# Kernel optimization log

Hardware: AMD Instinct MI355X
Metric: run time of the kernel (lower is better)

## Reference

```python
import jax, jax.numpy as jnp
import numpy as np

H = 16        # num_heads
LN_EPS = 1e-6

def _ln(x, w, b):
    mu = x.mean(-1, keepdims=True)
    var = ((x - mu) ** 2).mean(-1, keepdims=True)
    return (x - mu) * jax.lax.rsqrt(var + LN_EPS) * w + b

def setup_inputs():
    key = jax.random.key(0)
    ks = jax.random.split(key, 6)
    B, L, S, D = 2, 8192, 512, 1024
    std = 0.02
    return {
        "q_in": jax.random.normal(ks[0], (B, L, D), jnp.float32),
        "kv_in": jax.random.normal(ks[1], (B, S, D), jnp.float32),
        "qn_w": jnp.ones((D,), jnp.float32),
        "qn_b": jnp.zeros((D,), jnp.float32),
        "kvn_w": jnp.ones((D,), jnp.float32),
        "kvn_b": jnp.zeros((D,), jnp.float32),
        "Wq": jax.random.normal(ks[2], (D, D), jnp.float32) * std,
        "Wk": jax.random.normal(ks[3], (D, D), jnp.float32) * std,
        "Wv": jax.random.normal(ks[4], (D, D), jnp.float32) * std,
        "Wo": jax.random.normal(ks[5], (D, D), jnp.float32) * std,
        "bo": jnp.zeros((D,), jnp.float32),
        "gate": jnp.ones((1,), jnp.float32),
    }

def reference(q_in, kv_in, qn_w, qn_b, kvn_w, kvn_b, Wq, Wk, Wv, Wo, bo, gate):
    b, l, hid = q_in.shape
    s = kv_in.shape[1]
    d = hid // H
    scale = d ** -0.5
    q_x = _ln(q_in, qn_w, qn_b)
    kv_x = _ln(kv_in, kvn_w, kvn_b)
    # torch Linear: y = x @ W.T  (weights stored [out, in])
    q = (q_x @ Wq.T).reshape(b, l, H, d).transpose(0, 2, 1, 3)   # [b,H,l,d]
    k = (kv_x @ Wk.T).reshape(b, s, H, d).transpose(0, 2, 1, 3)  # [b,H,s,d]
    v = (kv_x @ Wv.T).reshape(b, s, H, d).transpose(0, 2, 1, 3)  # [b,H,s,d]
    logits = jnp.einsum('bhld,bhsd->bhls', q, k) * scale
    attn = jax.nn.softmax(logits, axis=-1)                       # [b,H,l,s]
    # no-grad diagnostics
    attn_d = jax.lax.stop_gradient(attn).astype(jnp.float32)
    ent_per_head = -(attn_d * jnp.log(attn_d + 1e-9)).sum(-1).mean(axis=(0, 2))  # [H]
    mean_entropy = ent_per_head.mean()
    head_entropy_std = ent_per_head.std()  # population std (unbiased=False)
    top_k = min(4, s)
    top_mass = jax.lax.top_k(attn_d, top_k)[0].sum(-1).mean()
    out = jnp.einsum('bhls,bhsd->bhld', attn, v)
    out = out.transpose(0, 2, 1, 3).reshape(b, l, hid)
    out = (out @ Wo.T + bo) * gate  # dropout=0 -> identity; gate broadcasts
    return (out, mean_entropy, head_entropy_std, top_mass, gate[0])
```

## Files before the change

kernel.cpp:

```cpp
#include <hip/hip_runtime.h>
#include <stdint.h>
#include <stddef.h>


typedef __attribute__((ext_vector_type(8))) short bf16x8;
typedef __attribute__((ext_vector_type(4))) float f32x4;
typedef __attribute__((ext_vector_type(16))) float f32x16;
typedef __attribute__((ext_vector_type(2))) unsigned int u32x2;

#define MFMA(a, b, c)   __builtin_amdgcn_mfma_f32_16x16x32_bf16((a), (b), (c), 0, 0, 0)
#define MFMA32(a, b, c) __builtin_amdgcn_mfma_f32_32x32x16_bf16((a), (b), (c), 0, 0, 0)
#define MED3(a, b, c)   __builtin_amdgcn_fmed3f((a), (b), (c))

__device__ __forceinline__ float bf2f(unsigned short u) {
  union { unsigned int ui; float f; } cv; cv.ui = ((unsigned int)u) << 16; return cv.f;
}
__device__ __forceinline__ unsigned short f2bf(float f) {
  union { float f; unsigned int ui; } cv; cv.f = f;
  unsigned int u = cv.ui;
  u = u + 0x7fffu + ((u >> 16) & 1u);
  return (unsigned short)(u >> 16);
}
__device__ __forceinline__ unsigned int pk2(float a, float b) {
  union { float f; unsigned int u; } ua, ub; ua.f = a; ub.f = b;
  return __builtin_amdgcn_perm(ub.u, ua.u, 0x07060302u);
}
__device__ __forceinline__ float ex2(float x) {
#if __has_builtin(__builtin_amdgcn_exp2f)
  return __builtin_amdgcn_exp2f(x);
#else
  float r; asm("v_exp_f32 %0, %1" : "=v"(r) : "v"(x)); return r;
#endif
}
__device__ __forceinline__ void pl32swap(unsigned int& a, unsigned int& b) {
#if __has_builtin(__builtin_amdgcn_permlane32_swap)
  u32x2 r = __builtin_amdgcn_permlane32_swap(a, b, false, false);
  a = r[0]; b = r[1];
#else
  asm volatile("v_permlane32_swap_b32 %0, %1" : "+v"(a), "+v"(b));
#endif
}
__device__ __forceinline__ bool is_fp32(const unsigned int* probe) {
  return probe[0] == 0x3F800000u;
}
__device__ __forceinline__ void gl2lds(const unsigned short* g, unsigned short* l) {
  __builtin_amdgcn_global_load_lds(
      (const __attribute__((address_space(1))) void*)(uintptr_t)g,
      (__attribute__((address_space(3))) void*)(unsigned int)(uintptr_t)l,
      16, 0, 0);
}

__device__ __forceinline__ size_t qf_addr(int qg, int d) {
  int b = qg >> 13, q = qg & 8191, h = d >> 6, dd = d & 63;
  int lane = (q & 31) | (((dd >> 3) & 1) << 5);
  return ((((size_t)(b * 16 + h) * 256 + (q >> 5)) * 4 + (dd >> 4)) * 64 + lane) * 8 + (dd & 7);
}
__device__ __forceinline__ size_t kf_addr(int r, int d) {
  int b = r >> 9, s = r & 511, h = d >> 6, dd = d & 63;
  int lane = (s & 31) | (((dd >> 3) & 1) << 5);
  return ((((size_t)(b * 16 + h) * 16 + (s >> 5)) * 4 + (dd >> 4)) * 64 + lane) * 8 + (dd & 7);
}
__device__ __forceinline__ size_t vf_addr(int r, int d) {
  int b = r >> 9, s = r & 511, h = d >> 6, dd = d & 63;
  int lane = (dd & 31) | (((s >> 3) & 1) << 5);
  return (((((size_t)(b * 16 + h) * 16 + (s >> 5)) * 2 + (dd >> 5)) * 2 + ((s >> 4) & 1)) * 64 + lane) * 8 + (s & 7);
}

__device__ __forceinline__ void ln_row_impl(
    bool f32, const void* __restrict__ xv, const void* __restrict__ wv,
    const void* __restrict__ bv, unsigned short* __restrict__ y,
    int row, int tid, float* rs, float* rs2)
{
  float v0, v1, v2, v3, w0, w1, w2, w3, b0, b1, b2, b3;
  if (f32) {
    float4 xr = *(const float4*)((const float*)xv + (size_t)row * 1024 + tid * 4);
    v0 = xr.x; v1 = xr.y; v2 = xr.z; v3 = xr.w;
    float4 wr = *(const float4*)((const float*)wv + tid * 4);
    w0 = wr.x; w1 = wr.y; w2 = wr.z; w3 = wr.w;
    float4 br = *(const float4*)((const float*)bv + tid * 4);
    b0 = br.x; b1 = br.y; b2 = br.z; b3 = br.w;
  } else {
    ushort4 xr = *(const ushort4*)((const unsigned short*)xv + (size_t)row * 1024 + tid * 4);
    v0 = bf2f(xr.x); v1 = bf2f(xr.y); v2 = bf2f(xr.z); v3 = bf2f(xr.w);
    ushort4 wr = *(const ushort4*)((const unsigned short*)wv + tid * 4);
    w0 = bf2f(wr.x); w1 = bf2f(wr.y); w2 = bf2f(wr.z); w3 = bf2f(wr.w);
    ushort4 br = *(const ushort4*)((const unsigned short*)bv + tid * 4);
    b0 = bf2f(br.x); b1 = bf2f(br.y); b2 = bf2f(br.z); b3 = bf2f(br.w);
  }
  float s  = v0 + v1 + v2 + v3;
  float s2 = v0*v0 + v1*v1 + v2*v2 + v3*v3;
  #pragma unroll
  for (int off = 32; off > 0; off >>= 1) {
    s  += __shfl_xor(s, off);
    s2 += __shfl_xor(s2, off);
  }
  if ((tid & 63) == 0) { rs[tid >> 6] = s; rs2[tid >> 6] = s2; }
  __syncthreads();
  s  = rs[0] + rs[1] + rs[2] + rs[3];
  s2 = rs2[0] + rs2[1] + rs2[2] + rs2[3];
  const float mean = s * (1.0f / 1024.0f);
  const float var  = s2 * (1.0f / 1024.0f) - mean * mean;
  const float rstd = 1.0f / sqrtf(var + 1e-6f);
  ushort4 o;
  o.x = f2bf((v0 - mean) * rstd * w0 + b0);
  o.y = f2bf((v1 - mean) * rstd * w1 + b1);
  o.z = f2bf((v2 - mean) * rstd * w2 + b2);
  o.w = f2bf((v3 - mean) * rstd * w3 + b3);
  *(ushort4*)(y + (size_t)row * 1024 + tid * 4) = o;
}

__global__ __launch_bounds__(256) void prep_all(
    const unsigned int* __restrict__ probe,
    const void* __restrict__ q_in, const void* __restrict__ qn_w,
    const void* __restrict__ qn_b, unsigned short* __restrict__ qx,
    const void* __restrict__ w0, const void* __restrict__ w1,
    const void* __restrict__ w2, const void* __restrict__ w3,
    unsigned short* __restrict__ wdst,
    const void* __restrict__ kv_in, const void* __restrict__ kvn_w,
    const void* __restrict__ kvn_b, unsigned short* __restrict__ kvx,
    const void* __restrict__ bo, const void* __restrict__ gate,
    unsigned short* __restrict__ bob, unsigned short* __restrict__ gateb,
    float* __restrict__ stats)
{
  __shared__ float rs[4], rs2[4];
  const bool f32 = is_fp32(probe);
  const int bx = blockIdx.x, tid = threadIdx.x;
  if (bx < 16384) {
    ln_row_impl(f32, q_in, qn_w, qn_b, qx, bx, tid, rs, rs2);
    return;
  }
  const int b2 = bx - 16384;
  if (b2 < 4096) {
    const int m = b2 >> 10;
    const void* src = (m == 0) ? w0 : (m == 1) ? w1 : (m == 2) ? w2 : w3;
    unsigned short* d = wdst + (size_t)m * 1048576;
    const int i = (b2 & 1023) * 1024 + tid * 4;
    ushort4 o;
    if (f32) {
      float4 v = *(const float4*)((const float*)src + i);
      o.x = f2bf(v.x); o.y = f2bf(v.y); o.z = f2bf(v.z); o.w = f2bf(v.w);
    } else {
      o = *(const ushort4*)((const unsigned short*)src + i);
    }
    *(ushort4*)(d + i) = o;
  } else if (b2 < 5120) {
    ln_row_impl(f32, kv_in, kvn_w, kvn_b, kvx, b2 - 4096, tid, rs, rs2);
  } else {
    ushort4 o;
    if (f32) {
      float4 v = *(const float4*)((const float*)bo + tid * 4);
      o.x = f2bf(v.x); o.y = f2bf(v.y); o.z = f2bf(v.z); o.w = f2bf(v.w);
    } else {
      o = *(const ushort4*)((const unsigned short*)bo + tid * 4);
    }
    *(ushort4*)(bob + tid * 4) = o;
    if (tid == 0)
      gateb[0] = f32 ? f2bf(((const float*)gate)[0]) : ((const unsigned short*)gate)[0];
    if (tid < 17) stats[tid] = 0.0f;
  }
}

template <int MODE>
__device__ __forceinline__ void gemm_core(
    const unsigned int* __restrict__ probe,
    const unsigned short* __restrict__ A, const unsigned short* __restrict__ B,
    void* __restrict__ Cv, int N, int K, int m0, int n0,
    const unsigned short* __restrict__ bias, const unsigned short* __restrict__ gate,
    unsigned short* As, unsigned short* Bs)
{
  const int tid = threadIdx.x;
  const int wave = tid >> 6, lane = tid & 63, ln = lane & 15, quad = lane >> 4;
  const int wm = (wave >> 1) * 64, wn = (wave & 1) * 64;
  f32x4 acc[4][4] = {};
  for (int k0 = 0; k0 < K; k0 += 64) {
    __syncthreads();
    #pragma unroll
    for (int i = 0; i < 4; i++) {
      int idx = tid + i * 256;
      int r = idx >> 3, ch = (idx & 7) * 8;
      gl2lds(A + (size_t)(m0 + r) * K + k0 + ch, As + r * 64 + ch);
      gl2lds(B + (size_t)(n0 + r) * K + k0 + ch, Bs + r * 64 + ch);
    }
    __syncthreads();
    #pragma unroll
    for (int kk = 0; kk < 64; kk += 32) {
      bf16x8 af[4], bfr[4];
      #pragma unroll
      for (int i = 0; i < 4; i++) {
        af[i]  = *(const bf16x8*)(As + (wm + i * 16 + ln) * 64 + kk + quad * 8);
        bfr[i] = *(const bf16x8*)(Bs + (wn + i * 16 + ln) * 64 + kk + quad * 8);
      }
      #pragma unroll
      for (int mi = 0; mi < 4; mi++)
        #pragma unroll
        for (int ni = 0; ni < 4; ni++)
          acc[mi][ni] = MFMA(af[mi], bfr[ni], acc[mi][ni]);
    }
  }
  const bool f32o = (MODE == 1) && is_fp32(probe);
  const float g = (MODE == 1) ? bf2f(gate[0]) : 1.0f;
  #pragma unroll
  for (int mi = 0; mi < 4; mi++) {
    #pragma unroll
    for (int ni = 0; ni < 4; ni++) {
      const int col = n0 + wn + ni * 16 + ln;
      const float badd = (MODE == 1) ? bf2f(bias[col]) : 0.0f;
      #pragma unroll
      for (int r = 0; r < 4; r++) {
        const int row = m0 + wm + mi * 16 + quad * 4 + r;
        const float val = (acc[mi][ni][r] + badd) * g;
        if (MODE == 1) {
          if (f32o) ((float*)Cv)[(size_t)row * N + col] = val;
          else ((unsigned short*)Cv)[(size_t)row * N + col] = f2bf(val);
        } else if (MODE == 2) {
          ((unsigned short*)Cv)[qf_addr(row, col)] = f2bf(val * 0.18033688f);
        } else {
          if (col < 1024) ((unsigned short*)Cv)[kf_addr(row, col)] = f2bf(val);
          else ((unsigned short*)Cv)[1048576 + vf_addr(row, col - 1024)] = f2bf(val);
        }
      }
    }
  }
}

template <int MODE>
__global__ __launch_bounds__(256, 3) void gemm_nt(
    const unsigned int* __restrict__ probe,
    const unsigned short* __restrict__ A, const unsigned short* __restrict__ B,
    void* __restrict__ Cv, int M, int N, int K,
    const unsigned short* __restrict__ bias, const unsigned short* __restrict__ gate)
{
  __shared__ unsigned short As[128 * 64];
  __shared__ unsigned short Bs[128 * 64];
  const int nbx = gridDim.x;
  const int nwg = nbx * gridDim.y;
  const int cpx = nwg >> 3;
  const int flat = blockIdx.y * nbx + blockIdx.x;
  const int swz = (flat & 7) * cpx + (flat >> 3);
  const int n0 = (swz % nbx) * 128;
  const int m0 = (swz / nbx) * 128;
  gemm_core<MODE>(probe, A, B, Cv, N, K, m0, n0, bias, gate, As, Bs);
}

__global__ __launch_bounds__(256, 3) void gemm_qkv(
    const unsigned int* __restrict__ probe,
    const unsigned short* __restrict__ qx, const unsigned short* __restrict__ kvx,
    const unsigned short* __restrict__ wcv,
    unsigned short* __restrict__ qfrag, unsigned short* __restrict__ kvfrag)
{
  __shared__ unsigned short As[128 * 64];
  __shared__ unsigned short Bs[128 * 64];
  const int flat = blockIdx.x;
  const int xcd = flat & 7, local = flat >> 3;
  if (local < 16) {
    const int id = xcd * 16 + local;
    gemm_core<5>(probe, kvx, wcv + 1048576, kvfrag, 2048, 1024,
                 (id >> 4) * 128, (id & 15) * 128, nullptr, nullptr, As, Bs);
  } else {
    const int id = xcd * 128 + (local - 16);
    gemm_core<2>(probe, qx, wcv, qfrag, 1024, 1024,
                 (id >> 3) * 128, (id & 7) * 128, nullptr, nullptr, As, Bs);
  }
}

#define TRK(T0, T1, T2, T3, L, SQ, IDX) {                                     \
    float x_ = S[IDX];                                                        \
    float o0 = T0, o1 = T1, o2 = T2;                                          \
    T0 = fmaxf(o0, x_); T1 = MED3(o0, o1, x_);                                \
    T2 = MED3(o1, o2, x_); T3 = MED3(o2, T3, x_);                             \
    float p_ = ex2(x_); L += p_; SQ = fmaf(p_, x_, SQ); S[IDX] = p_; }

#define MERGE4(A0, A1, A2, A3, B0, B1, B2, B3) {                              \
    float c0 = fmaxf(A0, B3), c1 = fmaxf(A1, B2);                             \
    float c2 = fmaxf(A2, B1), c3 = fmaxf(A3, B0);                             \
    float d0 = fmaxf(c0, c2), d2 = fminf(c0, c2);                             \
    float d1 = fmaxf(c1, c3), d3 = fminf(c1, c3);                             \
    A0 = fmaxf(d0, d1); A1 = fminf(d0, d1);                                   \
    A2 = fmaxf(d2, d3); A3 = fminf(d2, d3); }

__global__ __launch_bounds__(256, 3) void attn_kernel(
    const unsigned short* __restrict__ Qf, const unsigned short* __restrict__ Kf,
    const unsigned short* __restrict__ Vf, unsigned short* __restrict__ ctx,
    float* __restrict__ stats)
{
  __shared__ float red_e[4], red_t[4];
  const int tid = threadIdx.x;
  const int wave = tid >> 6, lane = tid & 63;
  const int qc = blockIdx.x & 63;
  const int bh = blockIdx.x >> 6;
  const int h = bh & 15, bb = bh >> 4;
  const int qt = qc * 4 + wave;

  const unsigned short* qfb = Qf + ((((size_t)bh * 256 + qt) * 4) * 64 + lane) * 8;
  const bf16x8 bq0 = *(const bf16x8*)(qfb);
  const bf16x8 bq1 = *(const bf16x8*)(qfb + 512);
  const bf16x8 bq2 = *(const bf16x8*)(qfb + 1024);
  const bf16x8 bq3 = *(const bf16x8*)(qfb + 1536);

  const unsigned short* kfb = Kf + ((size_t)bh * 64 * 64 + lane) * 8;
  const unsigned short* vfb = Vf + ((size_t)bh * 64 * 64 + lane) * 8;

  float l0 = 0.f, l1 = 0.f, l2 = 0.f, l3 = 0.f;
  float q0 = 0.f, q1 = 0.f, q2 = 0.f, q3 = 0.f;
  float ta0 = -1e30f, ta1 = -1e30f, ta2 = -1e30f, ta3 = -1e30f;
  float tb0 = -1e30f, tb1 = -1e30f, tb2 = -1e30f, tb3 = -1e30f;
  float tc0 = -1e30f, tc1 = -1e30f, tc2 = -1e30f, tc3 = -1e30f;
  float td0 = -1e30f, td1 = -1e30f, td2 = -1e30f, td3 = -1e30f;
  f32x16 Od0 = {}, Od1 = {};

  bf16x8 kf0 = *(const bf16x8*)(kfb);
  bf16x8 kf1 = *(const bf16x8*)(kfb + 512);
  bf16x8 kf2 = *(const bf16x8*)(kfb + 1024);
  bf16x8 kf3 = *(const bf16x8*)(kfb + 1536);

  for (int ch = 0; ch < 16; ch++) {
    const unsigned short* vp = vfb + (size_t)ch * 2048;
    const bf16x8 v00 = *(const bf16x8*)(vp);
    const bf16x8 v01 = *(const bf16x8*)(vp + 512);
    const bf16x8 v10 = *(const bf16x8*)(vp + 1024);
    const bf16x8 v11 = *(const bf16x8*)(vp + 1536);

    f32x16 S = {};
    __builtin_amdgcn_s_setprio(1);
    S = MFMA32(kf0, bq0, S);
    S = MFMA32(kf1, bq1, S);
    S = MFMA32(kf2, bq2, S);
    S = MFMA32(kf3, bq3, S);
    __builtin_amdgcn_s_setprio(0);

    {
      const unsigned short* kp = kfb + (size_t)(ch + 1) * 2048;
      kf0 = *(const bf16x8*)(kp);
      kf1 = *(const bf16x8*)(kp + 512);
      kf2 = *(const bf16x8*)(kp + 1024);
      kf3 = *(const bf16x8*)(kp + 1536);
    }

    TRK(ta0, ta1, ta2, ta3, l0, q0, 0)  TRK(tb0, tb1, tb2, tb3, l1, q1, 4)
    TRK(tc0, tc1, tc2, tc3, l2, q2, 8)  TRK(td0, td1, td2, td3, l3, q3, 12)
    TRK(ta0, ta1, ta2, ta3, l0, q0, 1)  TRK(tb0, tb1, tb2, tb3, l1, q1, 5)
    TRK(tc0, tc1, tc2, tc3, l2, q2, 9)  TRK(td0, td1, td2, td3, l3, q3, 13)
    TRK(ta0, ta1, ta2, ta3, l0, q0, 2)  TRK(tb0, tb1, tb2, tb3, l1, q1, 6)
    TRK(tc0, tc1, tc2, tc3, l2, q2, 10) TRK(td0, td1, td2, td3, l3, q3, 14)
    TRK(ta0, ta1, ta2, ta3, l0, q0, 3)  TRK(tb0, tb1, tb2, tb3, l1, q1, 7)
    TRK(tc0, tc1, tc2, tc3, l2, q2, 11) TRK(td0, td1, td2, td3, l3, q3, 15)

    unsigned int W0 = pk2(S[0],  S[1]),  W1 = pk2(S[2],  S[3]);
    unsigned int W2 = pk2(S[4],  S[5]),  W3 = pk2(S[6],  S[7]);
    unsigned int W4 = pk2(S[8],  S[9]),  W5 = pk2(S[10], S[11]);
    unsigned int W6 = pk2(S[12], S[13]), W7 = pk2(S[14], S[15]);
    pl32swap(W0, W2); pl32swap(W1, W3);
    pl32swap(W4, W6); pl32swap(W5, W7);
    union { unsigned int u[4]; bf16x8 v; } pb0, pb1;
    pb0.u[0] = W0; pb0.u[1] = W1; pb0.u[2] = W2; pb0.u[3] = W3;
    pb1.u[0] = W4; pb1.u[1] = W5; pb1.u[2] = W6; pb1.u[3] = W7;

    __builtin_amdgcn_s_setprio(1);
    Od0 = MFMA32(v00, pb0.v, Od0);
    Od0 = MFMA32(v01, pb1.v, Od0);
    Od1 = MFMA32(v10, pb0.v, Od1);
    Od1 = MFMA32(v11, pb1.v, Od1);
    __builtin_amdgcn_s_setprio(0);
  }

  MERGE4(ta0, ta1, ta2, ta3, tc0, tc1, tc2, tc3)
  MERGE4(tb0, tb1, tb2, tb3, td0, td1, td2, td3)
  MERGE4(ta0, ta1, ta2, ta3, tb0, tb1, tb2, tb3)
  float lq = (l0 + l1) + (l2 + l3);
  float sq = (q0 + q1) + (q2 + q3);
  lq += __shfl_xor(lq, 32);
  sq += __shfl_xor(sq, 32);
  {
    float o0 = __shfl_xor(ta0, 32), o1 = __shfl_xor(ta1, 32);
    float o2 = __shfl_xor(ta2, 32), o3 = __shfl_xor(ta3, 32);
    MERGE4(ta0, ta1, ta2, ta3, o0, o1, o2, o3)
  }
  const float invl = 1.0f / lq;
  float esum = 0.69314718f * (__log2f(lq) - sq * invl);
  float tsum = (ex2(ta0) + ex2(ta1) + ex2(ta2) + ex2(ta3)) * invl;
  #pragma unroll
  for (int off = 1; off < 64; off <<= 1) {
    esum += __shfl_xor(esum, off);
    tsum += __shfl_xor(tsum, off);
  }
  if (lane == 0) { red_e[wave] = esum * 0.5f; red_t[wave] = tsum * 0.5f; }
  __syncthreads();
  if (tid == 0) {
    atomicAdd(&stats[h],  red_e[0] + red_e[1] + red_e[2] + red_e[3]);
    atomicAdd(&stats[16], red_t[0] + red_t[1] + red_t[2] + red_t[3]);
  }

  const int qrow = lane & 31, hf = lane >> 5;
  unsigned short* cp = ctx + ((size_t)bb * 8192 + (size_t)qt * 32 + qrow) * 1024
                       + h * 64 + hf * 4;
  #pragma unroll
  for (int rg = 0; rg < 4; rg++) {
    ushort4 o;
    o.x = f2bf(Od0[rg * 4 + 0] * invl); o.y = f2bf(Od0[rg * 4 + 1] * invl);
    o.z = f2bf(Od0[rg * 4 + 2] * invl); o.w = f2bf(Od0[rg * 4 + 3] * invl);
    *(ushort4*)(cp + rg * 8) = o;
    o.x = f2bf(Od1[rg * 4 + 0] * invl); o.y = f2bf(Od1[rg * 4 + 1] * invl);
    o.z = f2bf(Od1[rg * 4 + 2] * invl); o.w = f2bf(Od1[rg * 4 + 3] * invl);
    *(ushort4*)(cp + 32 + rg * 8) = o;
  }
}

__global__ void finalize_kernel(const unsigned int* __restrict__ probe,
                                const float* __restrict__ stats,
                                const unsigned short* __restrict__ gateb,
                                void* __restrict__ out)
{
  if (threadIdx.x != 0) return;
  const bool f32 = is_fp32(probe);
  float e[16], s = 0.0f;
  for (int i = 0; i < 16; i++) { e[i] = stats[i] * (1.0f / 16384.0f); s += e[i]; }
  const float mean = s * (1.0f / 16.0f);
  float var = 0.0f;
  for (int i = 0; i < 16; i++) { float d = e[i] - mean; var += d * d; }
  var *= (1.0f / 16.0f);
  const float stdv = sqrtf(var);
  const float tm = stats[16] * (1.0f / 262144.0f);
  const float gv = bf2f(gateb[0]);
  if (f32) {
    float* t = (float*)out + 16777216;
    t[0] = mean; t[1] = stdv; t[2] = tm; t[3] = gv;
  } else {
    unsigned short* t = (unsigned short*)out + 16777216;
    t[0] = f2bf(mean); t[1] = f2bf(stdv); t[2] = f2bf(tm); t[3] = f2bf(gv);
  }
}

extern "C" void kernel_launch(void* const* d_in, const int* in_sizes, int n_in,
                              void* d_out, int out_size, void* d_ws, size_t ws_size,
                              hipStream_t stream)
{
  const void* q_in  = d_in[0];
  const void* kv_in = d_in[1];
  const unsigned int* probe = (const unsigned int*)d_in[2];
  const void* qn_w  = d_in[2];
  const void* qn_b  = d_in[3];
  const void* kvn_w = d_in[4];
  const void* kvn_b = d_in[5];
  const void* Wq    = d_in[6];
  const void* Wk    = d_in[7];
  const void* Wv    = d_in[8];
  const void* Wo    = d_in[9];
  const void* bo    = d_in[10];
  const void* gate  = d_in[11];

  unsigned short* ws    = (unsigned short*)d_ws;
  unsigned short* qx    = ws;
  unsigned short* kvx   = qx + 16777216;
  unsigned short* kfrag = kvx + 1048576;
  unsigned short* vfrag = kfrag + 1048576;
  unsigned short* wcv   = vfrag + 1048576;
  unsigned short* bob   = wcv + 4194304;
  unsigned short* gateb = bob + 1024;
  float* stats = (float*)(gateb + 8);
  unsigned short* qfrag = (unsigned short*)d_out;

  prep_all<<<21505, 256, 0, stream>>>(probe, q_in, qn_w, qn_b, qx,
                                      Wq, Wk, Wv, Wo, wcv,
                                      kv_in, kvn_w, kvn_b, kvx,
                                      bo, gate, bob, gateb, stats);
  gemm_qkv<<<1152, 256, 0, stream>>>(probe, qx, kvx, wcv, qfrag, kfrag);
  attn_kernel<<<2048, 256, 0, stream>>>(qfrag, kfrag, vfrag, qx , stats);
  gemm_nt<1><<<dim3(8, 128), 256, 0, stream>>>(probe, qx, wcv + 3145728, d_out,
                                               16384, 1024, 1024, bob, gateb);
  finalize_kernel<<<1, 64, 0, stream>>>(probe, stats, gateb, d_out);
}
```

Baseline: 324.7 us.

## Software-pipeline QK MFMA one chunk ahead of softmax in attention loop

The attention inner loop now computes the QK^T scores for the next KV chunk before running the softmax/stat tracking and PV MFMAs for the current chunk, using two alternating score accumulators. K fragments are prefetched two chunks ahead. This aims to overlap matrix-core work with the exp/top-k VALU work within a wave, at the cost of an extra 16-register accumulator that may raise register pressure under the 3-blocks-per-CU bound.

```diff
diff --git a/kernel.cpp b/kernel.cpp
--- a/kernel.cpp
+++ b/kernel.cpp
@@ -263,12 +263,12 @@
   }
 }
 
-#define TRK(T0, T1, T2, T3, L, SQ, IDX) {                                     \
-    float x_ = S[IDX];                                                        \
+#define TRK(SC, T0, T1, T2, T3, L, SQ, IDX) {                                 \
+    float x_ = (SC)[IDX];                                                     \
     float o0 = T0, o1 = T1, o2 = T2;                                          \
     T0 = fmaxf(o0, x_); T1 = MED3(o0, o1, x_);                                \
     T2 = MED3(o1, o2, x_); T3 = MED3(o2, T3, x_);                             \
-    float p_ = ex2(x_); L += p_; SQ = fmaf(p_, x_, SQ); S[IDX] = p_; }
+    float p_ = ex2(x_); L += p_; SQ = fmaf(p_, x_, SQ); (SC)[IDX] = p_; }
 
 #define MERGE4(A0, A1, A2, A3, B0, B1, B2, B3) {                              \
     float c0 = fmaxf(A0, B3), c1 = fmaxf(A1, B2);                             \
@@ -278,6 +278,48 @@
     A0 = fmaxf(d0, d1); A1 = fminf(d0, d1);                                   \
     A2 = fmaxf(d2, d3); A3 = fminf(d2, d3); }
 
+#define STAGE(SC, SN, CH) {                                                   \
+    { f32x16 z_ = {};                                                         \
+      __builtin_amdgcn_s_setprio(1);                                          \
+      SN = MFMA32(kf0, bq0, z_);                                              \
+      SN = MFMA32(kf1, bq1, SN);                                              \
+      SN = MFMA32(kf2, bq2, SN);                                              \
+      SN = MFMA32(kf3, bq3, SN);                                              \
+      __builtin_amdgcn_s_setprio(0); }                                        \
+    { const unsigned short* kp_ = kfb + (size_t)((CH) + 2) * 2048;            \
+      kf0 = *(const bf16x8*)(kp_);                                            \
+      kf1 = *(const bf16x8*)(kp_ + 512);                                      \
+      kf2 = *(const bf16x8*)(kp_ + 1024);                                     \
+      kf3 = *(const bf16x8*)(kp_ + 1536); }                                   \
+    const unsigned short* vp_##SC = vfb + (size_t)(CH) * 2048;                \
+    const bf16x8 v00 = *(const bf16x8*)(vp_##SC);                             \
+    const bf16x8 v01 = *(const bf16x8*)(vp_##SC + 512);                       \
+    const bf16x8 v10 = *(const bf16x8*)(vp_##SC + 1024);                      \
+    const bf16x8 v11 = *(const bf16x8*)(vp_##SC + 1536);                      \
+    TRK(SC, ta0, ta1, ta2, ta3, l0, q0, 0)  TRK(SC, tb0, tb1, tb2, tb3, l1, q1, 4)  \
+    TRK(SC, tc0, tc1, tc2, tc3, l2, q2, 8)  TRK(SC, td0, td1, td2, td3, l3, q3, 12) \
+    TRK(SC, ta0, ta1, ta2, ta3, l0, q0, 1)  TRK(SC, tb0, tb1, tb2, tb3, l1, q1, 5)  \
+    TRK(SC, tc0, tc1, tc2, tc3, l2, q2, 9)  TRK(SC, td0, td1, td2, td3, l3, q3, 13) \
+    TRK(SC, ta0, ta1, ta2, ta3, l0, q0, 2)  TRK(SC, tb0, tb1, tb2, tb3, l1, q1, 6)  \
+    TRK(SC, tc0, tc1, tc2, tc3, l2, q2, 10) TRK(SC, td0, td1, td2, td3, l3, q3, 14) \
+    TRK(SC, ta0, ta1, ta2, ta3, l0, q0, 3)  TRK(SC, tb0, tb1, tb2, tb3, l1, q1, 7)  \
+    TRK(SC, tc0, tc1, tc2, tc3, l2, q2, 11) TRK(SC, td0, td1, td2, td3, l3, q3, 15) \
+    unsigned int W0 = pk2((SC)[0],  (SC)[1]),  W1 = pk2((SC)[2],  (SC)[3]);   \
+    unsigned int W2 = pk2((SC)[4],  (SC)[5]),  W3 = pk2((SC)[6],  (SC)[7]);   \
+    unsigned int W4 = pk2((SC)[8],  (SC)[9]),  W5 = pk2((SC)[10], (SC)[11]);  \
+    unsigned int W6 = pk2((SC)[12], (SC)[13]), W7 = pk2((SC)[14], (SC)[15]);  \
+    pl32swap(W0, W2); pl32swap(W1, W3);                                       \
+    pl32swap(W4, W6); pl32swap(W5, W7);                                       \
+    union { unsigned int u[4]; bf16x8 v; } pb0, pb1;                          \
+    pb0.u[0] = W0; pb0.u[1] = W1; pb0.u[2] = W2; pb0.u[3] = W3;               \
+    pb1.u[0] = W4; pb1.u[1] = W5; pb1.u[2] = W6; pb1.u[3] = W7;               \
+    __builtin_amdgcn_s_setprio(1);                                            \
+    Od0 = MFMA32(v00, pb0.v, Od0);                                            \
+    Od0 = MFMA32(v01, pb1.v, Od0);                                            \
+    Od1 = MFMA32(v10, pb0.v, Od1);                                            \
+    Od1 = MFMA32(v11, pb1.v, Od1);                                            \
+    __builtin_amdgcn_s_setprio(0); }
+
 __global__ __launch_bounds__(256, 3) void attn_kernel(
     const unsigned short* __restrict__ Qf, const unsigned short* __restrict__ Kf,
     const unsigned short* __restrict__ Vf, unsigned short* __restrict__ ctx,
@@ -312,55 +354,22 @@
   bf16x8 kf1 = *(const bf16x8*)(kfb + 512);
   bf16x8 kf2 = *(const bf16x8*)(kfb + 1024);
   bf16x8 kf3 = *(const bf16x8*)(kfb + 1536);
-
-  for (int ch = 0; ch < 16; ch++) {
-    const unsigned short* vp = vfb + (size_t)ch * 2048;
-    const bf16x8 v00 = *(const bf16x8*)(vp);
-    const bf16x8 v01 = *(const bf16x8*)(vp + 512);
-    const bf16x8 v10 = *(const bf16x8*)(vp + 1024);
-    const bf16x8 v11 = *(const bf16x8*)(vp + 1536);
-
-    f32x16 S = {};
-    __builtin_amdgcn_s_setprio(1);
-    S = MFMA32(kf0, bq0, S);
-    S = MFMA32(kf1, bq1, S);
-    S = MFMA32(kf2, bq2, S);
-    S = MFMA32(kf3, bq3, S);
-    __builtin_amdgcn_s_setprio(0);
-
-    {
-      const unsigned short* kp = kfb + (size_t)(ch + 1) * 2048;
-      kf0 = *(const bf16x8*)(kp);
-      kf1 = *(const bf16x8*)(kp + 512);
-      kf2 = *(const bf16x8*)(kp + 1024);
-      kf3 = *(const bf16x8*)(kp + 1536);
-    }
-
-    TRK(ta0, ta1, ta2, ta3, l0, q0, 0)  TRK(tb0, tb1, tb2, tb3, l1, q1, 4)
-    TRK(tc0, tc1, tc2, tc3, l2, q2, 8)  TRK(td0, td1, td2, td3, l3, q3, 12)
-    TRK(ta0, ta1, ta2, ta3, l0, q0, 1)  TRK(tb0, tb1, tb2, tb3, l1, q1, 5)
-    TRK(tc0, tc1, tc2, tc3, l2, q2, 9)  TRK(td0, td1, td2, td3, l3, q3, 13)
-    TRK(ta0, ta1, ta2, ta3, l0, q0, 2)  TRK(tb0, tb1, tb2, tb3, l1, q1, 6)
-    TRK(tc0, tc1, tc2, tc3, l2, q2, 10) TRK(td0, td1, td2, td3, l3, q3, 14)
-    TRK(ta0, ta1, ta2, ta3, l0, q0, 3)  TRK(tb0, tb1, tb2, tb3, l1, q1, 7)
-    TRK(tc0, tc1, tc2, tc3, l2, q2, 11) TRK(td0, td1, td2, td3, l3, q3, 15)
-
-    unsigned int W0 = pk2(S[0],  S[1]),  W1 = pk2(S[2],  S[3]);
-    unsigned int W2 = pk2(S[4],  S[5]),  W3 = pk2(S[6],  S[7]);
-    unsigned int W4 = pk2(S[8],  S[9]),  W5 = pk2(S[10], S[11]);
-    unsigned int W6 = pk2(S[12], S[13]), W7 = pk2(S[14], S[15]);
-    pl32swap(W0, W2); pl32swap(W1, W3);
-    pl32swap(W4, W6); pl32swap(W5, W7);
-    union { unsigned int u[4]; bf16x8 v; } pb0, pb1;
-    pb0.u[0] = W0; pb0.u[1] = W1; pb0.u[2] = W2; pb0.u[3] = W3;
-    pb1.u[0] = W4; pb1.u[1] = W5; pb1.u[2] = W6; pb1.u[3] = W7;
-
-    __builtin_amdgcn_s_setprio(1);
-    Od0 = MFMA32(v00, pb0.v, Od0);
-    Od0 = MFMA32(v01, pb1.v, Od0);
-    Od1 = MFMA32(v10, pb0.v, Od1);
-    Od1 = MFMA32(v11, pb1.v, Od1);
-    __builtin_amdgcn_s_setprio(0);
+  f32x16 SA, SB;
+  {
+    f32x16 z_ = {};
+    SA = MFMA32(kf0, bq0, z_);
+    SA = MFMA32(kf1, bq1, SA);
+    SA = MFMA32(kf2, bq2, SA);
+    SA = MFMA32(kf3, bq3, SA);
+  }
+  kf0 = *(const bf16x8*)(kfb + 2048);
+  kf1 = *(const bf16x8*)(kfb + 2560);
+  kf2 = *(const bf16x8*)(kfb + 3072);
+  kf3 = *(const bf16x8*)(kfb + 3584);
+
+  for (int ch = 0; ch < 16; ch += 2) {
+    STAGE(SA, SB, ch)
+    STAGE(SB, SA, ch + 1)
   }
 
   MERGE4(ta0, ta1, ta2, ta3, tc0, tc1, tc2, tc3)
```

Measured after the change: 347.4 us. +7.0%, slower.

## Halve top-k tracker chains, raise occupancy to 4 blocks, swizzle block order

Applied to the files above, without the earlier changes.

Cuts the per-lane top-4 tracking from four independent chains to two, which frees about 16 registers. The launch bound moves from 3 to 4 blocks per CU to use that headroom. Block indices are also swizzled so consecutive blocks map to different (batch, head) pairs, spreading K/V traffic across the L2/XCDs. In exchange, the longer dependency chains in the tracking code reduce instruction-level parallelism in the softmax section.

```diff
diff --git a/kernel.cpp b/kernel.cpp
--- a/kernel.cpp
+++ b/kernel.cpp
@@ -278,7 +278,7 @@
     A0 = fmaxf(d0, d1); A1 = fminf(d0, d1);                                   \
     A2 = fmaxf(d2, d3); A3 = fminf(d2, d3); }
 
-__global__ __launch_bounds__(256, 3) void attn_kernel(
+__global__ __launch_bounds__(256, 4) void attn_kernel(
     const unsigned short* __restrict__ Qf, const unsigned short* __restrict__ Kf,
     const unsigned short* __restrict__ Vf, unsigned short* __restrict__ ctx,
     float* __restrict__ stats)
@@ -286,8 +286,10 @@
   __shared__ float red_e[4], red_t[4];
   const int tid = threadIdx.x;
   const int wave = tid >> 6, lane = tid & 63;
-  const int qc = blockIdx.x & 63;
-  const int bh = blockIdx.x >> 6;
+  const int bid = (int)blockIdx.x;
+  const int swzb = (bid & 7) * 256 + (bid >> 3);
+  const int qc = swzb & 63;
+  const int bh = swzb >> 6;
   const int h = bh & 15, bb = bh >> 4;
   const int qt = qc * 4 + wave;
 
@@ -300,12 +302,10 @@
   const unsigned short* kfb = Kf + ((size_t)bh * 64 * 64 + lane) * 8;
   const unsigned short* vfb = Vf + ((size_t)bh * 64 * 64 + lane) * 8;
 
-  float l0 = 0.f, l1 = 0.f, l2 = 0.f, l3 = 0.f;
-  float q0 = 0.f, q1 = 0.f, q2 = 0.f, q3 = 0.f;
+  float la = 0.f, lb = 0.f;
+  float sa = 0.f, sb = 0.f;
   float ta0 = -1e30f, ta1 = -1e30f, ta2 = -1e30f, ta3 = -1e30f;
   float tb0 = -1e30f, tb1 = -1e30f, tb2 = -1e30f, tb3 = -1e30f;
-  float tc0 = -1e30f, tc1 = -1e30f, tc2 = -1e30f, tc3 = -1e30f;
-  float td0 = -1e30f, td1 = -1e30f, td2 = -1e30f, td3 = -1e30f;
   f32x16 Od0 = {}, Od1 = {};
 
   bf16x8 kf0 = *(const bf16x8*)(kfb);
@@ -336,14 +336,14 @@
       kf3 = *(const bf16x8*)(kp + 1536);
     }
 
-    TRK(ta0, ta1, ta2, ta3, l0, q0, 0)  TRK(tb0, tb1, tb2, tb3, l1, q1, 4)
-    TRK(tc0, tc1, tc2, tc3, l2, q2, 8)  TRK(td0, td1, td2, td3, l3, q3, 12)
-    TRK(ta0, ta1, ta2, ta3, l0, q0, 1)  TRK(tb0, tb1, tb2, tb3, l1, q1, 5)
-    TRK(tc0, tc1, tc2, tc3, l2, q2, 9)  TRK(td0, td1, td2, td3, l3, q3, 13)
-    TRK(ta0, ta1, ta2, ta3, l0, q0, 2)  TRK(tb0, tb1, tb2, tb3, l1, q1, 6)
-    TRK(tc0, tc1, tc2, tc3, l2, q2, 10) TRK(td0, td1, td2, td3, l3, q3, 14)
-    TRK(ta0, ta1, ta2, ta3, l0, q0, 3)  TRK(tb0, tb1, tb2, tb3, l1, q1, 7)
-    TRK(tc0, tc1, tc2, tc3, l2, q2, 11) TRK(td0, td1, td2, td3, l3, q3, 15)
+    TRK(ta0, ta1, ta2, ta3, la, sa, 0)  TRK(tb0, tb1, tb2, tb3, lb, sb, 8)
+    TRK(ta0, ta1, ta2, ta3, la, sa, 1)  TRK(tb0, tb1, tb2, tb3, lb, sb, 9)
+    TRK(ta0, ta1, ta2, ta3, la, sa, 2)  TRK(tb0, tb1, tb2, tb3, lb, sb, 10)
+    TRK(ta0, ta1, ta2, ta3, la, sa, 3)  TRK(tb0, tb1, tb2, tb3, lb, sb, 11)
+    TRK(ta0, ta1, ta2, ta3, la, sa, 4)  TRK(tb0, tb1, tb2, tb3, lb, sb, 12)
+    TRK(ta0, ta1, ta2, ta3, la, sa, 5)  TRK(tb0, tb1, tb2, tb3, lb, sb, 13)
+    TRK(ta0, ta1, ta2, ta3, la, sa, 6)  TRK(tb0, tb1, tb2, tb3, lb, sb, 14)
+    TRK(ta0, ta1, ta2, ta3, la, sa, 7)  TRK(tb0, tb1, tb2, tb3, lb, sb, 15)
 
     unsigned int W0 = pk2(S[0],  S[1]),  W1 = pk2(S[2],  S[3]);
     unsigned int W2 = pk2(S[4],  S[5]),  W3 = pk2(S[6],  S[7]);
@@ -363,11 +363,9 @@
     __builtin_amdgcn_s_setprio(0);
   }
 
-  MERGE4(ta0, ta1, ta2, ta3, tc0, tc1, tc2, tc3)
-  MERGE4(tb0, tb1, tb2, tb3, td0, td1, td2, td3)
   MERGE4(ta0, ta1, ta2, ta3, tb0, tb1, tb2, tb3)
-  float lq = (l0 + l1) + (l2 + l3);
-  float sq = (q0 + q1) + (q2 + q3);
+  float lq = la + lb;
+  float sq = sa + sb;
   lq += __shfl_xor(lq, 32);
   sq += __shfl_xor(sq, 32);
   {
```

Measured after the change: 324.0 us. No clear change (-0.2%).

## Use 256x256-tile pipelined GEMM for Q projection and output projection

Applied to the files above, without the earlier changes.

Adds a new 512-thread GEMM kernel with 256x256 output tiles, swizzled LDS layout, double-buffered global-to-LDS staging interleaved with MFMA phases, and s_setprio/sched barriers. It replaces the 128x128 kernel for the large Q projection and the Wo projection. The fused QKV launch is split into a separate KV GEMM launch using the old core, which is now specialized to the KV epilogue. Larger tiles raise arithmetic intensity and cut LDS/global reloads, but they leave only 256 workgroups at one per CU and add an extra kernel launch.

```diff
diff --git a/kernel.cpp b/kernel.cpp
--- a/kernel.cpp
+++ b/kernel.cpp
@@ -11,6 +11,8 @@
 #define MFMA(a, b, c)   __builtin_amdgcn_mfma_f32_16x16x32_bf16((a), (b), (c), 0, 0, 0)
 #define MFMA32(a, b, c) __builtin_amdgcn_mfma_f32_32x32x16_bf16((a), (b), (c), 0, 0, 0)
 #define MED3(a, b, c)   __builtin_amdgcn_fmed3f((a), (b), (c))
+#define SBAR()  __builtin_amdgcn_s_barrier()
+#define SCHED0() __builtin_amdgcn_sched_barrier(0)
 
 __device__ __forceinline__ float bf2f(unsigned short u) {
   union { unsigned int ui; float f; } cv; cv.ui = ((unsigned int)u) << 16; return cv.f;
@@ -197,27 +199,17 @@
           acc[mi][ni] = MFMA(af[mi], bfr[ni], acc[mi][ni]);
     }
   }
-  const bool f32o = (MODE == 1) && is_fp32(probe);
-  const float g = (MODE == 1) ? bf2f(gate[0]) : 1.0f;
   #pragma unroll
   for (int mi = 0; mi < 4; mi++) {
     #pragma unroll
     for (int ni = 0; ni < 4; ni++) {
       const int col = n0 + wn + ni * 16 + ln;
-      const float badd = (MODE == 1) ? bf2f(bias[col]) : 0.0f;
       #pragma unroll
       for (int r = 0; r < 4; r++) {
         const int row = m0 + wm + mi * 16 + quad * 4 + r;
-        const float val = (acc[mi][ni][r] + badd) * g;
-        if (MODE == 1) {
-          if (f32o) ((float*)Cv)[(size_t)row * N + col] = val;
-          else ((unsigned short*)Cv)[(size_t)row * N + col] = f2bf(val);
-        } else if (MODE == 2) {
-          ((unsigned short*)Cv)[qf_addr(row, col)] = f2bf(val * 0.18033688f);
-        } else {
-          if (col < 1024) ((unsigned short*)Cv)[kf_addr(row, col)] = f2bf(val);
-          else ((unsigned short*)Cv)[1048576 + vf_addr(row, col - 1024)] = f2bf(val);
-        }
+        const float val = acc[mi][ni][r];
+        if (col < 1024) ((unsigned short*)Cv)[kf_addr(row, col)] = f2bf(val);
+        else ((unsigned short*)Cv)[1048576 + vf_addr(row, col - 1024)] = f2bf(val);
       }
     }
   }
@@ -242,24 +234,117 @@
   gemm_core<MODE>(probe, A, B, Cv, N, K, m0, n0, bias, gate, As, Bs);
 }
 
-__global__ __launch_bounds__(256, 3) void gemm_qkv(
+#define STG256(mat, row0, base, h, kt) {                                      \
+    _Pragma("unroll")                                                         \
+    for (int i_ = 0; i_ < 2; i_++) {                                          \
+      int rl_ = (h) * 128 + i_ * 64 + (tid >> 3);                             \
+      int cb_ = (tid & 7) ^ (((rl_ >> 2) & 1) << 1);                          \
+      gl2lds(mat + (size_t)((row0) + rl_) * K + (kt) * 64 + cb_ * 8,          \
+             lds + (base) + rl_ * 64 + (tid & 7) * 8);                        \
+    } }
+#define RDA256(abase, MH, KK) {                                               \
+    _Pragma("unroll")                                                         \
+    for (int f_ = 0; f_ < 4; f_++) {                                          \
+      int rl_ = wm + (MH) * 64 + f_ * 16 + ln;                                \
+      af[f_] = *(const bf16x8*)(lds + (abase) + rl_ * 64 +                    \
+                 (((KK) + quad * 8) ^ (((rl_ >> 2) & 1) << 4)));              \
+    } }
+#define RDB256(bbase, KK) {                                                   \
+    _Pragma("unroll")                                                         \
+    for (int f_ = 0; f_ < 4; f_++) {                                          \
+      int rl_ = wn + f_ * 16 + ln;                                            \
+      bf[f_] = *(const bf16x8*)(lds + (bbase) + rl_ * 64 +                    \
+                 (((KK) + quad * 8) ^ (((rl_ >> 2) & 1) << 4)));              \
+    } }
+#define MM16(MH) {                                                            \
+    __builtin_amdgcn_s_setprio(1);                                            \
+    _Pragma("unroll")                                                         \
+    for (int mi_ = 0; mi_ < 4; mi_++)                                         \
+      _Pragma("unroll")                                                       \
+      for (int ni_ = 0; ni_ < 4; ni_++)                                       \
+        acc[(MH) * 4 + mi_][ni_] = MFMA(af[mi_], bf[ni_], acc[(MH)*4+mi_][ni_]); \
+    __builtin_amdgcn_s_setprio(0); }
+#define VM2() asm volatile("s_waitcnt vmcnt(2)" ::: "memory")
+
+template <int MODE>
+__global__ __launch_bounds__(512, 1) void gemm256(
     const unsigned int* __restrict__ probe,
-    const unsigned short* __restrict__ qx, const unsigned short* __restrict__ kvx,
-    const unsigned short* __restrict__ wcv,
-    unsigned short* __restrict__ qfrag, unsigned short* __restrict__ kvfrag)
-{
-  __shared__ unsigned short As[128 * 64];
-  __shared__ unsigned short Bs[128 * 64];
-  const int flat = blockIdx.x;
-  const int xcd = flat & 7, local = flat >> 3;
-  if (local < 16) {
-    const int id = xcd * 16 + local;
-    gemm_core<5>(probe, kvx, wcv + 1048576, kvfrag, 2048, 1024,
-                 (id >> 4) * 128, (id & 15) * 128, nullptr, nullptr, As, Bs);
-  } else {
-    const int id = xcd * 128 + (local - 16);
-    gemm_core<2>(probe, qx, wcv, qfrag, 1024, 1024,
-                 (id >> 3) * 128, (id & 7) * 128, nullptr, nullptr, As, Bs);
+    const unsigned short* __restrict__ A, const unsigned short* __restrict__ Bm,
+    void* __restrict__ Cv, int M, int N, int K,
+    const unsigned short* __restrict__ bias, const unsigned short* __restrict__ gate)
+{
+  __shared__ unsigned short lds[65536];
+  const int tid = threadIdx.x;
+  const int wave = tid >> 6, lane = tid & 63, ln = lane & 15, quad = lane >> 4;
+  const int wm = (wave >> 2) * 128, wn = (wave & 3) * 64;
+
+  const int nbx = gridDim.x;
+  const int nwg = nbx * gridDim.y;
+  const int cpx = nwg >> 3;
+  const int flat = blockIdx.y * nbx + blockIdx.x;
+  const int swz = (flat & 7) * cpx + (flat >> 3);
+  const int n0 = (swz % nbx) * 256;
+  const int m0 = (swz / nbx) * 256;
+
+  f32x4 acc[8][4] = {};
+  const int NT = K >> 6;
+
+  STG256(Bm, n0, 32768, 0, 0) STG256(Bm, n0, 32768, 1, 0)
+  STG256(A,  m0, 0,     0, 0) STG256(A,  m0, 0,     1, 0)
+  STG256(Bm, n0, 49152, 0, 1)
+  VM2();
+  SBAR(); SCHED0();
+
+  for (int t = 0; t < NT; t += 2) {
+    bf16x8 af[4], bf[4];
+    const int t2 = (t + 2 < NT) ? t + 2 : 0;
+    const int t3 = (t + 3 < NT) ? t + 3 : 0;
+    RDA256(0, 0, 0) RDB256(32768, 0)
+    STG256(Bm, n0, 49152, 1, t + 1)
+    SBAR(); SCHED0(); MM16(0) SBAR(); SCHED0();
+    RDA256(0, 1, 0)
+    STG256(A, m0, 16384, 0, t + 1)
+    SBAR(); SCHED0(); MM16(1) SBAR(); SCHED0();
+    RDA256(0, 0, 32) RDB256(32768, 32)
+    STG256(A, m0, 16384, 1, t + 1)
+    SBAR(); SCHED0(); MM16(0) SBAR(); SCHED0();
+    RDA256(0, 1, 32)
+    STG256(Bm, n0, 32768, 0, t2)
+    SBAR(); SCHED0(); MM16(1) VM2(); SBAR(); SCHED0();
+    RDA256(16384, 0, 0) RDB256(49152, 0)
+    STG256(Bm, n0, 32768, 1, t2)
+    SBAR(); SCHED0(); MM16(0) SBAR(); SCHED0();
+    RDA256(16384, 1, 0)
+    STG256(A, m0, 0, 0, t2)
+    SBAR(); SCHED0(); MM16(1) SBAR(); SCHED0();
+    RDA256(16384, 0, 32) RDB256(49152, 32)
+    STG256(A, m0, 0, 1, t2)
+    SBAR(); SCHED0(); MM16(0) SBAR(); SCHED0();
+    RDA256(16384, 1, 32)
+    STG256(Bm, n0, 49152, 0, t3)
+    SBAR(); SCHED0(); MM16(1) VM2(); SBAR(); SCHED0();
+  }
+
+  const bool f32o = (MODE == 1) && is_fp32(probe);
+  const float g = (MODE == 1) ? bf2f(gate[0]) : 1.0f;
+  #pragma unroll
+  for (int mf = 0; mf < 8; mf++) {
+    #pragma unroll
+    for (int nf = 0; nf < 4; nf++) {
+      const int col = n0 + wn + nf * 16 + ln;
+      const float badd = (MODE == 1) ? bf2f(bias[col]) : 0.0f;
+      #pragma unroll
+      for (int r = 0; r < 4; r++) {
+        const int row = m0 + wm + mf * 16 + quad * 4 + r;
+        const float val = (acc[mf][nf][r] + badd) * g;
+        if (MODE == 1) {
+          if (f32o) ((float*)Cv)[(size_t)row * N + col] = val;
+          else ((unsigned short*)Cv)[(size_t)row * N + col] = f2bf(val);
+        } else {
+          ((unsigned short*)Cv)[qf_addr(row, col)] = f2bf(val * 0.18033688f);
+        }
+      }
+    }
   }
 }
 
@@ -463,9 +548,12 @@
                                       Wq, Wk, Wv, Wo, wcv,
                                       kv_in, kvn_w, kvn_b, kvx,
                                       bo, gate, bob, gateb, stats);
-  gemm_qkv<<<1152, 256, 0, stream>>>(probe, qx, kvx, wcv, qfrag, kfrag);
+  gemm_nt<5><<<dim3(16, 8), 256, 0, stream>>>(probe, kvx, wcv + 1048576, kfrag,
+                                              1024, 2048, 1024, nullptr, nullptr);
+  gemm256<2><<<dim3(4, 64), 512, 0, stream>>>(probe, qx, wcv, qfrag,
+                                              16384, 1024, 1024, nullptr, nullptr);
   attn_kernel<<<2048, 256, 0, stream>>>(qfrag, kfrag, vfrag, qx , stats);
-  gemm_nt<1><<<dim3(8, 128), 256, 0, stream>>>(probe, qx, wcv + 3145728, d_out,
-                                               16384, 1024, 1024, bob, gateb);
+  gemm256<1><<<dim3(4, 64), 512, 0, stream>>>(probe, qx, wcv + 3145728, d_out,
+                                              16384, 1024, 1024, bob, gateb);
   finalize_kernel<<<1, 64, 0, stream>>>(probe, stats, gateb, d_out);
 }
```

After: 318.7 us. Within noise of the previous version (-1.9%).
